# Kernel optimization log

Measured on AMD Instinct MI355X. Metric: run time of the kernel, lower is better.

The kernel has to match this reference:

```python
import jax, jax.numpy as jnp
import numpy as np

ALPHA = 0.2  # LeakyReLU negative slope
NEG_INF = -1e9


def _build_mask(N, seq_len, seg_len):
    # mask: [4, N, N], matches the torch construction exactly
    eyeN = jnp.eye(N, dtype=jnp.float32)
    m0 = eyeN
    m1 = jnp.zeros((N, N), jnp.float32)
    m1 = m1.at[seq_len:seq_len + seg_len, seq_len:seq_len + seg_len].set(
        1.0 - jnp.eye(seg_len, dtype=jnp.float32))
    m2 = jnp.zeros((N, N), jnp.float32)
    m2 = m2.at[:seq_len, seq_len:seq_len + seg_len].set(1.0)
    m2 = m2.at[seq_len:seq_len + seg_len, :seq_len].set(1.0)
    m3 = jnp.zeros((N, N), jnp.float32)
    m3 = m3.at[seq_len + seg_len:, :seq_len].set(1.0)
    m3 = m3.at[:seq_len, seq_len + seg_len:].set(1.0)
    return jnp.stack([m0, m1, m2, m3], axis=0)


def setup_inputs() -> dict:
    key = jax.random.key(0)
    k_in, k_adj, k_W, k_a1, k_a2 = jax.random.split(key, 5)
    B, N, d_in, d_out = 8, 1024, 256, 256
    inp = jax.random.normal(k_in, (B, N, d_in), dtype=jnp.float32)
    adj = jax.random.randint(k_adj, (B, N, N), 0, 2, dtype=jnp.int32)
    # xavier_uniform with gain=1.414
    def xavier(k, shape, gain=1.414):
        fan_out, fan_in = shape[0], shape[-1]
        bound = gain * np.sqrt(6.0 / (fan_in + fan_out))
        return jax.random.uniform(k, shape, jnp.float32, -bound, bound)
    W = xavier(k_W, (d_out, d_in))          # Linear(in, out, bias=False): y = x @ W.T
    a1 = xavier(k_a1, (4, d_out))           # four Linear(out, 1) weights stacked
    a2 = xavier(k_a2, (4, d_out))
    return {"input": inp, "adj": adj, "W": W, "a1": a1, "a2": a2,
            "seq_len": 512, "seg_len": 256, "gaz_len": 256}


def reference(input, adj, W, a1, a2, seq_len, seg_len, gaz_len):
    B, N, _ = input.shape
    h = jnp.einsum('bnd,od->bno', input, W)            # [B, N, out]
    s1 = jnp.einsum('bno,ko->kbn', h, a1)              # [4, B, N]
    s2 = jnp.einsum('bno,ko->kbn', h, a2)              # [4, B, N]
    e = s1[..., :, None] + s2[..., None, :]            # [4, B, N, N]
    e = jnp.where(e > 0, e, ALPHA * e)                 # LeakyReLU
    mask = _build_mask(N, seq_len, seg_len)            # [4, N, N]
    attention = jnp.einsum('kbij,kij->bij', e, mask)   # weighted sum of 4 score maps
    attention = jnp.where(adj == 0, NEG_INF, attention)
    attention = jax.nn.softmax(attention, axis=2)
    # dropout skipped (eval mode / deterministic reference)
    h_prime = jnp.matmul(attention, h)                 # [B, N, out]
    return jax.nn.elu(h_prime)                         # concat=True path
```

## Files before the change

kernel.cpp:

```cpp
#include <hip/hip_runtime.h>
#include <hip/hip_bf16.h>

#define B_ 8
#define N_ 1024
#define D_ 256
#define M_ (B_ * N_)

typedef __attribute__((ext_vector_type(8))) short bf16x8;
typedef __attribute__((ext_vector_type(8))) unsigned short u16x8;
typedef __attribute__((ext_vector_type(4))) float f32x4;

__device__ __forceinline__ unsigned short f2bf(float f) {
    unsigned int u = __float_as_uint(f);
    u += 0x7fffu + ((u >> 16) & 1u);
    return (unsigned short)(u >> 16);
}
__device__ __forceinline__ unsigned int cvtpk(float lo, float hi) {
    unsigned int r;
    asm("v_cvt_pk_bf16_f32 %0, %1, %2" : "=v"(r) : "v"(lo), "v"(hi));
    return r;
}
__device__ __forceinline__ bf16x8 load8_f32_bf(const float* __restrict__ p) {
    const float4* q = (const float4*)p;
    float4 u = q[0], v = q[1];
    union { unsigned int u4[4]; bf16x8 v8; } c;
    c.u4[0] = cvtpk(u.x, u.y); c.u4[1] = cvtpk(u.z, u.w);
    c.u4[2] = cvtpk(v.x, v.y); c.u4[3] = cvtpk(v.z, v.w);
    return c.v8;
}

__global__ __launch_bounds__(512) void k_hgemm(const float* __restrict__ x,
        const float* __restrict__ W,
        const float* __restrict__ a1, const float* __restrict__ a2,
        unsigned short* __restrict__ hT,
        float* __restrict__ s1, float* __restrict__ s2) {
    __shared__ unsigned short xs[32 * 256];
    __shared__ unsigned short tls[8][32][40];
    __shared__ float spart[8][32][9];
    const int tid = threadIdx.x;
    const int wslot = tid >> 6, lane = tid & 63;
    const int mt = (blockIdx.x & 7) * 32 + (blockIdx.x >> 3);
    const int m0 = mt * 32, n0 = wslot * 32;
    char* xc = (char*)xs;

    {
        const int row = tid >> 4, colg = (tid & 15) * 16;
        const float4* xp = (const float4*)(x + (m0 + row) * D_ + colg);
        float4 f0 = xp[0], f1 = xp[1], f2 = xp[2], f3 = xp[3];
        union { unsigned int u4[8]; u16x8 v8[2]; } c;
        c.u4[0] = cvtpk(f0.x, f0.y); c.u4[1] = cvtpk(f0.z, f0.w);
        c.u4[2] = cvtpk(f1.x, f1.y); c.u4[3] = cvtpk(f1.z, f1.w);
        c.u4[4] = cvtpk(f2.x, f2.y); c.u4[5] = cvtpk(f2.z, f2.w);
        c.u4[6] = cvtpk(f3.x, f3.y); c.u4[7] = cvtpk(f3.z, f3.w);
        const int base = row * 512 + colg * 2, sw = (row & 7) << 4;
        *(u16x8*)(xc + ((base) ^ sw))      = c.v8[0];
        *(u16x8*)(xc + ((base + 16) ^ sw)) = c.v8[1];
    }
    __syncthreads();

    const int r = lane & 15, kg = lane >> 4;
    const int sw = (r & 7) << 4;
    const int abase0 = r * 512, abase1 = (16 + r) * 512;
    const float* wb0 = W + (n0 + r) * D_ + kg * 8;
    const float* wb1 = wb0 + 16 * D_;
    f32x4 z = {0.f, 0.f, 0.f, 0.f};
    f32x4 acc00 = z, acc01 = z, acc10 = z, acc11 = z;
    bf16x8 nb0 = load8_f32_bf(wb0);
    bf16x8 nb1 = load8_f32_bf(wb1);
    #pragma unroll
    for (int d0 = 0; d0 < D_; d0 += 32) {
        const int kb = (d0 + kg * 8) * 2;
        bf16x8 a0 = *(const bf16x8*)(xc + ((abase0 + kb) ^ sw));
        bf16x8 a1f = *(const bf16x8*)(xc + ((abase1 + kb) ^ sw));
        bf16x8 b0 = nb0, b1 = nb1;
        if (d0 + 32 < D_) {
            nb0 = load8_f32_bf(wb0 + d0 + 32);
            nb1 = load8_f32_bf(wb1 + d0 + 32);
        }
        acc00 = __builtin_amdgcn_mfma_f32_16x16x32_bf16(a0, b0, acc00, 0, 0, 0);
        acc01 = __builtin_amdgcn_mfma_f32_16x16x32_bf16(a0, b1, acc01, 0, 0, 0);
        acc10 = __builtin_amdgcn_mfma_f32_16x16x32_bf16(a1f, b0, acc10, 0, 0, 0);
        acc11 = __builtin_amdgcn_mfma_f32_16x16x32_bf16(a1f, b1, acc11, 0, 0, 0);
    }
    const int col = lane & 15, rb = (lane >> 4) * 4;
    f32x4 accs[2][2] = {{acc00, acc01}, {acc10, acc11}};
    #pragma unroll
    for (int rt = 0; rt < 2; ++rt)
      #pragma unroll
      for (int ct = 0; ct < 2; ++ct)
        #pragma unroll
        for (int q = 0; q < 4; ++q)
            tls[wslot][rt * 16 + rb + q][ct * 16 + col] = f2bf(accs[rt][ct][q]);
    __syncthreads();

    {
        bf16x8 bfr = {0, 0, 0, 0, 0, 0, 0, 0};
        if (r < 8) {
            const float* ap = (r < 4 ? a1 + r * D_ : a2 + (r - 4) * D_) + n0 + kg * 8;
            bfr = load8_f32_bf(ap);
        }
        bf16x8 af0 = *(const bf16x8*)&tls[wslot][r][kg * 8];
        bf16x8 af1 = *(const bf16x8*)&tls[wslot][16 + r][kg * 8];
        f32x4 s0 = __builtin_amdgcn_mfma_f32_16x16x32_bf16(af0, bfr, z, 0, 0, 0);
        f32x4 s1v = __builtin_amdgcn_mfma_f32_16x16x32_bf16(af1, bfr, z, 0, 0, 0);
        if (col < 8) {
            #pragma unroll
            for (int q = 0; q < 4; ++q) {
                spart[wslot][rb + q][col] = s0[q];
                spart[wslot][16 + rb + q][col] = s1v[q];
            }
        }
    }

    const int bb = m0 >> 10, nbase = m0 & 1023;
    const int ol = lane >> 1, nh = lane & 1;
    unsigned short vv[16];
    #pragma unroll
    for (int q2 = 0; q2 < 16; ++q2) vv[q2] = tls[wslot][nh * 16 + q2][ol];
    u16x8 lo, hi;
    #pragma unroll
    for (int q2 = 0; q2 < 8; ++q2) { lo[q2] = vv[q2]; hi[q2] = vv[8 + q2]; }
    unsigned short* dst = hT + ((size_t)(bb * D_ + n0 + ol)) * N_ + nbase + nh * 16;
    *(u16x8*)dst = lo;
    *(u16x8*)(dst + 8) = hi;

    __syncthreads();
    if (tid < 256) {
        const int row = tid >> 3, s = tid & 7;
        float v = 0.f;
        #pragma unroll
        for (int wv = 0; wv < 8; ++wv) v += spart[wv][row][s];
        if (s < 4) s1[s * M_ + m0 + row] = v;
        else       s2[(s - 4) * M_ + m0 + row] = v;
    }
}

__global__ __launch_bounds__(512) void k_fused(const int* __restrict__ adj,
        const float* __restrict__ s1, const float* __restrict__ s2,
        const unsigned short* __restrict__ hT, float* __restrict__ out) {
    __shared__ unsigned short Pe[32 * 1024];
    __shared__ float invl[32];
    const int b  = blockIdx.x & 7;
    const int i0 = (blockIdx.x >> 3) << 5;
    const int tid = threadIdx.x;

    const int w = tid >> 6, lane = tid & 63;
    const int r = lane & 15, kg = lane >> 4;
    const int o0 = w << 5;
    const unsigned short* hTb = hT + (((size_t)b) << 18);
    const unsigned short* pb0 = hTb + (o0 + r) * N_ + kg * 8;
    const unsigned short* pb1 = pb0 + 16 * N_;
    bf16x8 c00 = *(const bf16x8*)pb0;
    bf16x8 c10 = *(const bf16x8*)pb1;
    bf16x8 c01 = *(const bf16x8*)(pb0 + 32);
    bf16x8 c11 = *(const bf16x8*)(pb1 + 32);

    {
        const int ir = tid >> 4, tj = tid & 15;
        const int i = i0 + ir;
        const int gr = b * N_ + i;
        const float s1i0 = s1[0 * M_ + gr], s1i1 = s1[1 * M_ + gr];
        const float s1i2 = s1[2 * M_ + gr], s1i3 = s1[3 * M_ + gr];
        float zbA, zbB, zbC; int koA, koB, koC;
        if (i < 512)      { zbA = 0.f;  koA = -1;     zbB = s1i2; koB = 2 * M_; zbC = s1i3; koC = 3 * M_; }
        else if (i < 768) { zbA = s1i2; koA = 2 * M_; zbB = s1i1; koB = 1 * M_; zbC = 0.f;  koC = -1;     }
        else              { zbA = s1i3; koA = 3 * M_; zbB = 0.f;  koB = -1;     zbC = 0.f;  koC = -1;     }
        float dval; { float t = s1i0 + s2[b * N_ + i]; dval = fmaxf(t, 0.2f * t); }
        const int* arow = adj + (size_t)gr * N_;
        const float* s2b = s2 + b * N_;
        float cbase[8]; int cko[8];
        #pragma unroll
        for (int c = 0; c < 8; ++c) {
            cbase[c] = c < 4 ? zbA : (c < 6 ? zbB : zbC);
            cko[c]   = c < 4 ? koA : (c < 6 ? koB : koC);
        }
        float lsum = 0.f;
        int4 pa0 = *(const int4*)(arow + tj * 8);
        int4 pa1 = *(const int4*)(arow + tj * 8 + 4);
        const float* sp0 = s2b + (cko[0] < 0 ? 0 : cko[0]) + tj * 8;
        float4 pv0 = *(const float4*)sp0;
        float4 pv1 = *(const float4*)(sp0 + 4);
        #pragma unroll
        for (int c = 0; c < 8; ++c) {
            const int j0 = c * 128 + tj * 8;
            const float base = cbase[c]; const int ko = cko[c];
            const int4 a0 = pa0, a1v = pa1;
            const float4 v0 = pv0, v1 = pv1;
            if (c < 7) {
                const int j0n = (c + 1) * 128 + tj * 8;
                pa0 = *(const int4*)(arow + j0n);
                pa1 = *(const int4*)(arow + j0n + 4);
                const float* sp = s2b + (cko[c + 1] < 0 ? 0 : cko[c + 1]) + j0n;
                pv0 = *(const float4*)sp; pv1 = *(const float4*)(sp + 4);
            }
            const float sv[8] = {v0.x, v0.y, v0.z, v0.w, v1.x, v1.y, v1.z, v1.w};
            const int   av[8] = {a0.x, a0.y, a0.z, a0.w, a1v.x, a1v.y, a1v.z, a1v.w};
            float evv[8];
            #pragma unroll
            for (int q = 0; q < 8; ++q) {
                const int j = j0 + q;
                float att;
                if (ko >= 0) { float t = base + sv[q]; att = fmaxf(t, 0.2f * t); }
                else att = 0.f;
                if (j == i) att = dval;
                const float ev = (av[q] == 0) ? 0.f : __expf(att);
                lsum += ev;
                evv[q] = ev;
            }
            union { unsigned int u4[4]; u16x8 v8; } c8;
            c8.u4[0] = cvtpk(evv[0], evv[1]); c8.u4[1] = cvtpk(evv[2], evv[3]);
            c8.u4[2] = cvtpk(evv[4], evv[5]); c8.u4[3] = cvtpk(evv[6], evv[7]);
            *(u16x8*)((char*)Pe + ((ir * 2048 + j0 * 2) ^ ((ir & 7) << 4))) = c8.v8;
        }
        lsum += __shfl_xor(lsum, 1, 64);
        lsum += __shfl_xor(lsum, 2, 64);
        lsum += __shfl_xor(lsum, 4, 64);
        lsum += __shfl_xor(lsum, 8, 64);
        if (tj == 0) invl[ir] = 1.f / lsum;
    }
    __syncthreads();

    f32x4 z = {0.f, 0.f, 0.f, 0.f};
    f32x4 acc00 = z, acc01 = z, acc10 = z, acc11 = z;
    const char* Pc = (const char*)Pe;
    const int sw0 = (r & 7) << 4;
    const int base0 = r * 2048, base1 = (16 + r) * 2048;
    #pragma unroll 2
    for (int k0 = 0; k0 < N_; k0 += 64) {
        int kb = (k0 + kg * 8) * 2;
        bf16x8 a0 = *(const bf16x8*)(Pc + ((base0 + kb) ^ sw0));
        bf16x8 a1f = *(const bf16x8*)(Pc + ((base1 + kb) ^ sw0));
        bf16x8 b0 = c00, b1 = c10;
        if (k0 + 64 < N_) {
            c00 = *(const bf16x8*)(pb0 + k0 + 64);
            c10 = *(const bf16x8*)(pb1 + k0 + 64);
        }
        acc00 = __builtin_amdgcn_mfma_f32_16x16x32_bf16(a0, b0, acc00, 0, 0, 0);
        acc01 = __builtin_amdgcn_mfma_f32_16x16x32_bf16(a0, b1, acc01, 0, 0, 0);
        acc10 = __builtin_amdgcn_mfma_f32_16x16x32_bf16(a1f, b0, acc10, 0, 0, 0);
        acc11 = __builtin_amdgcn_mfma_f32_16x16x32_bf16(a1f, b1, acc11, 0, 0, 0);
        kb = (k0 + 32 + kg * 8) * 2;
        a0 = *(const bf16x8*)(Pc + ((base0 + kb) ^ sw0));
        a1f = *(const bf16x8*)(Pc + ((base1 + kb) ^ sw0));
        b0 = c01; b1 = c11;
        if (k0 + 96 < N_) {
            c01 = *(const bf16x8*)(pb0 + k0 + 96);
            c11 = *(const bf16x8*)(pb1 + k0 + 96);
        }
        acc00 = __builtin_amdgcn_mfma_f32_16x16x32_bf16(a0, b0, acc00, 0, 0, 0);
        acc01 = __builtin_amdgcn_mfma_f32_16x16x32_bf16(a0, b1, acc01, 0, 0, 0);
        acc10 = __builtin_amdgcn_mfma_f32_16x16x32_bf16(a1f, b0, acc10, 0, 0, 0);
        acc11 = __builtin_amdgcn_mfma_f32_16x16x32_bf16(a1f, b1, acc11, 0, 0, 0);
    }
    const int col = lane & 15, rb = (lane >> 4) << 2;
    f32x4 accs[2][2] = {{acc00, acc01}, {acc10, acc11}};
    #pragma unroll
    for (int rt = 0; rt < 2; ++rt) {
        #pragma unroll
        for (int q = 0; q < 4; ++q) {
            const int il = rt * 16 + rb + q;
            const float sc = invl[il];
            #pragma unroll
            for (int ct = 0; ct < 2; ++ct) {
                float v = accs[rt][ct][q] * sc;
                v = v > 0.f ? v : (__expf(v) - 1.f);
                out[((size_t)(b * N_ + i0 + il)) * D_ + o0 + ct * 16 + col] = v;
            }
        }
    }
}

extern "C" void kernel_launch(void* const* d_in, const int* in_sizes, int n_in,
                              void* d_out, int out_size, void* d_ws, size_t ws_size,
                              hipStream_t stream) {
    const float* x   = (const float*)d_in[0];
    const int*   adj = (const int*)d_in[1];
    const float* W   = (const float*)d_in[2];
    const float* a1  = (const float*)d_in[3];
    const float* a2  = (const float*)d_in[4];
    float* out = (float*)d_out;

    char* ws = (char*)d_ws;
    unsigned short* hT = (unsigned short*)ws;
    float* s1 = (float*)(ws + (4u << 20));
    float* s2 = (float*)(ws + (4u << 20) + (128u << 10));

    hipLaunchKernelGGL(k_hgemm, dim3(256), dim3(512), 0, stream, x, W, a1, a2, hT, s1, s2);
    hipLaunchKernelGGL(k_fused, dim3(256), dim3(512), 0, stream, adj, s1, s2, hT, out);
}
```

Measured before the change: 39.20 us.

## Pack adjacency into bitmask in projection kernel and consume bits in fused softmax

```diff
diff --git a/kernel.cpp b/kernel.cpp
--- a/kernel.cpp
+++ b/kernel.cpp
@@ -32,8 +32,10 @@
 __global__ __launch_bounds__(512) void k_hgemm(const float* __restrict__ x,
         const float* __restrict__ W,
         const float* __restrict__ a1, const float* __restrict__ a2,
+        const int* __restrict__ adj,
         unsigned short* __restrict__ hT,
-        float* __restrict__ s1, float* __restrict__ s2) {
+        float* __restrict__ s1, float* __restrict__ s2,
+        unsigned long long* __restrict__ mask) {
     __shared__ unsigned short xs[32 * 256];
     __shared__ unsigned short tls[8][32][40];
     __shared__ float spart[8][32][9];
@@ -133,9 +135,36 @@
         if (s < 4) s1[s * M_ + m0 + row] = v;
         else       s2[(s - 4) * M_ + m0 + row] = v;
     }
-}
-
-__global__ __launch_bounds__(512) void k_fused(const int* __restrict__ adj,
+
+    {
+        const int wrow = m0 + wslot * 4;
+        #pragma unroll
+        for (int rp = 0; rp < 2; ++rp) {
+            int a0v[16], a1v[16];
+            const int* r0p = adj + (size_t)(wrow + rp * 2) * N_ + lane;
+            const int* r1p = r0p + N_;
+            #pragma unroll
+            for (int seg = 0; seg < 16; ++seg) {
+                a0v[seg] = __builtin_nontemporal_load(r0p + seg * 64);
+                a1v[seg] = __builtin_nontemporal_load(r1p + seg * 64);
+            }
+            unsigned long long w0 = 0, w1 = 0;
+            #pragma unroll
+            for (int seg = 0; seg < 16; ++seg) {
+                unsigned long long b0 = __ballot(a0v[seg] != 0);
+                unsigned long long b1 = __ballot(a1v[seg] != 0);
+                if (lane == seg) { w0 = b0; w1 = b1; }
+            }
+            if (lane < 16) {
+                mask[(size_t)(wrow + rp * 2) * 16 + lane]     = w0;
+                mask[(size_t)(wrow + rp * 2 + 1) * 16 + lane] = w1;
+            }
+        }
+    }
+}
+
+__global__ __launch_bounds__(512) void k_fused(
+        const unsigned long long* __restrict__ mask,
         const float* __restrict__ s1, const float* __restrict__ s2,
         const unsigned short* __restrict__ hT, float* __restrict__ out) {
     __shared__ unsigned short Pe[32 * 1024];
@@ -161,49 +190,46 @@
         const int gr = b * N_ + i;
         const float s1i0 = s1[0 * M_ + gr], s1i1 = s1[1 * M_ + gr];
         const float s1i2 = s1[2 * M_ + gr], s1i3 = s1[3 * M_ + gr];
-        float zbA, zbB, zbC; int koA, koB, koC;
-        if (i < 512)      { zbA = 0.f;  koA = -1;     zbB = s1i2; koB = 2 * M_; zbC = s1i3; koC = 3 * M_; }
-        else if (i < 768) { zbA = s1i2; koA = 2 * M_; zbB = s1i1; koB = 1 * M_; zbC = 0.f;  koC = -1;     }
-        else              { zbA = s1i3; koA = 3 * M_; zbB = 0.f;  koB = -1;     zbC = 0.f;  koC = -1;     }
+        float base; int ko;
+        if (i < 512) {
+            if (tj < 8)       { base = 0.f;  ko = -1; }
+            else if (tj < 12) { base = s1i2; ko = 2 * M_; }
+            else              { base = s1i3; ko = 3 * M_; }
+        } else if (i < 768) {
+            if (tj < 8)       { base = s1i2; ko = 2 * M_; }
+            else if (tj < 12) { base = s1i1; ko = 1 * M_; }
+            else              { base = 0.f;  ko = -1; }
+        } else {
+            if (tj < 8)       { base = s1i3; ko = 3 * M_; }
+            else              { base = 0.f;  ko = -1; }
+        }
         float dval; { float t = s1i0 + s2[b * N_ + i]; dval = fmaxf(t, 0.2f * t); }
-        const int* arow = adj + (size_t)gr * N_;
-        const float* s2b = s2 + b * N_;
-        float cbase[8]; int cko[8];
-        #pragma unroll
-        for (int c = 0; c < 8; ++c) {
-            cbase[c] = c < 4 ? zbA : (c < 6 ? zbB : zbC);
-            cko[c]   = c < 4 ? koA : (c < 6 ? koB : koC);
-        }
+        const unsigned long long m = mask[(size_t)gr * 16 + tj];
+        const float* s2k = s2 + b * N_ + (ko < 0 ? 0 : ko) + tj * 64;
         float lsum = 0.f;
-        int4 pa0 = *(const int4*)(arow + tj * 8);
-        int4 pa1 = *(const int4*)(arow + tj * 8 + 4);
-        const float* sp0 = s2b + (cko[0] < 0 ? 0 : cko[0]) + tj * 8;
-        float4 pv0 = *(const float4*)sp0;
-        float4 pv1 = *(const float4*)(sp0 + 4);
-        #pragma unroll
-        for (int c = 0; c < 8; ++c) {
-            const int j0 = c * 128 + tj * 8;
-            const float base = cbase[c]; const int ko = cko[c];
-            const int4 a0 = pa0, a1v = pa1;
-            const float4 v0 = pv0, v1 = pv1;
-            if (c < 7) {
-                const int j0n = (c + 1) * 128 + tj * 8;
-                pa0 = *(const int4*)(arow + j0n);
-                pa1 = *(const int4*)(arow + j0n + 4);
-                const float* sp = s2b + (cko[c + 1] < 0 ? 0 : cko[c + 1]) + j0n;
-                pv0 = *(const float4*)sp; pv1 = *(const float4*)(sp + 4);
-            }
-            const float sv[8] = {v0.x, v0.y, v0.z, v0.w, v1.x, v1.y, v1.z, v1.w};
-            const int   av[8] = {a0.x, a0.y, a0.z, a0.w, a1v.x, a1v.y, a1v.z, a1v.w};
+        #pragma unroll
+        for (int qq = 0; qq < 8; ++qq) {
+            const int q8 = (qq + tj) & 7;
+            const int j0 = tj * 64 + q8 * 8;
+            float sv[8];
+            if (ko >= 0) {
+                float4 v0 = *(const float4*)(s2k + q8 * 8);
+                float4 v1 = *(const float4*)(s2k + q8 * 8 + 4);
+                sv[0] = v0.x; sv[1] = v0.y; sv[2] = v0.z; sv[3] = v0.w;
+                sv[4] = v1.x; sv[5] = v1.y; sv[6] = v1.z; sv[7] = v1.w;
+            } else {
+                #pragma unroll
+                for (int q = 0; q < 8; ++q) sv[q] = 0.f;
+            }
+            const unsigned int mb = (unsigned int)(m >> (q8 * 8)) & 0xffu;
             float evv[8];
             #pragma unroll
             for (int q = 0; q < 8; ++q) {
                 const int j = j0 + q;
-                float att;
-                if (ko >= 0) { float t = base + sv[q]; att = fmaxf(t, 0.2f * t); }
-                else att = 0.f;
+                float t = base + sv[q];
+                float att = fmaxf(t, 0.2f * t);
                 if (j == i) att = dval;
-                const float ev = (av[q] == 0) ? 0.f : __expf(att);
+                const float ev = ((mb >> q) & 1u) ? __expf(att) : 0.f;
                 lsum += ev;
                 evv[q] = ev;
             }
@@ -264,7 +290,8 @@
             for (int ct = 0; ct < 2; ++ct) {
                 float v = accs[rt][ct][q] * sc;
                 v = v > 0.f ? v : (__expf(v) - 1.f);
-                out[((size_t)(b * N_ + i0 + il)) * D_ + o0 + ct * 16 + col] = v;
+                __builtin_nontemporal_store(v,
+                    &out[((size_t)(b * N_ + i0 + il)) * D_ + o0 + ct * 16 + col]);
             }
         }
     }
@@ -284,7 +311,8 @@
     unsigned short* hT = (unsigned short*)ws;
     float* s1 = (float*)(ws + (4u << 20));
     float* s2 = (float*)(ws + (4u << 20) + (128u << 10));
-
-    hipLaunchKernelGGL(k_hgemm, dim3(256), dim3(512), 0, stream, x, W, a1, a2, hT, s1, s2);
-    hipLaunchKernelGGL(k_fused, dim3(256), dim3(512), 0, stream, adj, s1, s2, hT, out);
-}
+    unsigned long long* mask = (unsigned long long*)(ws + (4u << 20) + (512u << 10));
+
+    hipLaunchKernelGGL(k_hgemm, dim3(256), dim3(512), 0, stream, x, W, a1, a2, adj, hT, s1, s2, mask);
+    hipLaunchKernelGGL(k_fused, dim3(256), dim3(512), 0, stream, mask, s1, s2, hT, out);
+}
```

Result: slower. 40.81 us (+4.1%).
